# Kernel tuning notes

Hardware: AMD Instinct MI355X
Metric: run time of the kernel (lower is better)

## Reference

```python
import jax, jax.numpy as jnp
import numpy as np

BSZ = 2048
L = 64            # sequence length, power of 2
D = 15            # symbol_repr_size
NC = 10           # n_classes; embedding row NC is the 'inf' token
TREE_LEN = 2 * L - 1  # next_power_of_2(L)*2 - 1


def rms_norm(x):
    # x / (sqrt(mean(x^2, -1) + 1e-6) + 1e-6)
    return x / (jnp.sqrt(jnp.mean(x * x, axis=-1, keepdims=True) + 1e-6) + 1e-6)


def setup_inputs() -> dict:
    key = jax.random.key(0)
    k1, k2, k3, k4, k5 = jax.random.split(key, 5)
    x = jax.random.randint(k1, (BSZ, L), 0, NC)
    q = jnp.sort(jax.random.randint(k2, (BSZ, 2), 0, L), axis=1)  # low <= high
    query_low, query_high = q[:, 0], q[:, 1]
    emb = jax.random.normal(k3, (NC + 1, D), dtype=jnp.float32)
    W_lin = jax.random.normal(k4, (NC, D), dtype=jnp.float32) * 0.26   # ~1/sqrt(D)
    W_rule = jax.random.normal(k5, (2, D * D), dtype=jnp.float32) * 0.066  # ~1/D
    return {"emb": emb, "W_lin": W_lin, "W_rule": W_rule,
            "x": x, "query_low": query_low, "query_high": query_high}


def reference(emb, W_lin, W_rule, x, query_low, query_high):
    def combine(a, b):
        # outer product [b, D, D] -> rule linear (225 -> 2) -> softmax mix
        inp = jnp.einsum('bi,bj->bij', a, b).reshape(a.shape[0], -1)
        alpha = jax.nn.softmax(inp @ W_rule.T, axis=-1)  # [b, 2]
        return alpha[:, :1] * a + alpha[:, 1:] * b

    def build(trees, lst, low, high, pos):
        # recursive segment-tree build; low/high/pos are static Python ints
        if low == high:
            return rms_norm(trees.at[:, pos, :].set(lst[:, low, :]))
        mid = (low + high) // 2
        trees = build(trees, lst, low, mid, 2 * pos + 1)
        trees = build(trees, lst, mid + 1, high, 2 * pos + 2)
        mix = combine(trees[:, 2 * pos + 1], trees[:, 2 * pos + 2])
        return rms_norm(trees.at[:, pos, :].set(mix))

    inf_raw = emb[NC]  # raw inf token used inside query (no rms_norm in torch)

    def query(trees, returns, low, high, pos):
        if pos >= TREE_LEN:
            return returns
        f = returns.dtype
        mA = ((query_low <= low) & (query_high >= high)).astype(f)[:, None]
        returns = mA * trees[:, pos] + (1 - mA) * returns
        mB = ((query_low > high) | (query_high < low)).astype(f)[:, None]
        returns = mB * inf_raw[None, :] + (1 - mB) * returns
        mC = (1 - mA) * (1 - mB)
        mid = (low + high) // 2
        a1 = query(trees, returns, low, mid, 2 * pos + 1)
        a2 = query(trees, returns, mid + 1, high, 2 * pos + 2)
        new = combine(a1, a2)
        return rms_norm(mC * new + (1 - mC) * returns)

    h = rms_norm(emb[x])                              # [BSZ, L, D]
    inf_n = rms_norm(emb[NC][None, None, :])          # normalized inf token
    trees = jnp.broadcast_to(inf_n, (BSZ, TREE_LEN, D)) + jnp.zeros((), emb.dtype)
    trees = build(trees, h, 0, L - 1, 0)              # [BSZ, TREE_LEN, D]
    returns = jnp.zeros((BSZ, D), dtype=emb.dtype)
    returns = query(trees, returns, 0, L - 1, 0)      # [BSZ, D]
    return returns @ W_lin.T                          # [BSZ, NC]
```

## Files before the change

### kernel.cpp

```cpp
#include <hip/hip_runtime.h>
#include <math.h>

#define DD 15
#define DP 20
#define LL 64
#define NCC 10
#define TL 127

__device__ __forceinline__ float dpp_xor1(float x) {
    return __int_as_float(__builtin_amdgcn_update_dpp(0, __float_as_int(x), 177, 0xF, 0xF, true));
}
__device__ __forceinline__ float dpp_xor2(float x) {
    return __int_as_float(__builtin_amdgcn_update_dpp(0, __float_as_int(x), 78, 0xF, 0xF, true));
}
__device__ __forceinline__ float swz_xor4(float x) {
    return __int_as_float(__builtin_amdgcn_ds_swizzle(__float_as_int(x), 0x101F));
}

__device__ __forceinline__ float fast_rcp(float x)  { return __builtin_amdgcn_rcpf(x); }
__device__ __forceinline__ float fast_sqrt(float x) { return __builtin_amdgcn_sqrtf(x); }

__device__ __forceinline__ void combine8(const float (*tree)[DP], const float w[4][DD],
                                         int k, int qr, int u, int p,
                                         float& v0, float& v1, float& inv)
{
    const float* Lrow = &tree[2 * p + 1][0];
    const float* Rrow = &tree[2 * p + 2][0];
    float4 R0 = ((const float4*)Rrow)[0];
    float4 R1 = ((const float4*)Rrow)[1];
    float4 R2 = ((const float4*)Rrow)[2];
    float4 R3 = ((const float4*)Rrow)[3];
    float4 Aq = ((const float4*)Lrow)[qr];
    float Bv[DD] = {R0.x,R0.y,R0.z,R0.w, R1.x,R1.y,R1.z,R1.w,
                    R2.x,R2.y,R2.z,R2.w, R3.x,R3.y,R3.z};
    float Av[4] = {Aq.x, Aq.y, Aq.z, Aq.w};

    float acc = 0.f;
    #pragma unroll
    for (int ri = 0; ri < 4; ++ri) {
        float d0 = 0.f;
        #pragma unroll
        for (int j = 0; j < DD; ++j) d0 = fmaf(w[ri][j], Bv[j], d0);
        acc = fmaf(Av[ri], d0, acc);
    }
    acc += dpp_xor2(acc);
    acc += swz_xor4(acc);
    float oth = dpp_xor1(acc);
    float mx = fmaxf(acc, oth);
    float es = __expf(acc - mx), eo = __expf(oth - mx);
    float rs = fast_rcp(es + eo);
    float aS = es * rs, aO = eo * rs;
    float a0 = (k == 0) ? aS : aO;
    float a1 = (k == 0) ? aO : aS;

    float2 lm = ((const float2*)Lrow)[u];
    float2 rm = ((const float2*)Rrow)[u];
    v0 = a0 * lm.x + a1 * rm.x;
    v1 = a0 * lm.y + a1 * rm.y;
    float ss = v0 * v0 + v1 * v1;
    ss += dpp_xor1(ss);
    ss += dpp_xor2(ss);
    ss += swz_xor4(ss);
    inv = fast_rcp(fast_sqrt(ss * (1.0f / DD) + 1e-6f) + 1e-6f);
}

template<int LVL, bool QUERY>
__device__ __forceinline__ void do_level(float (*tree)[DP], const float (*nemb)[DP],
                                         const float w[4][DD], int t, int ql, int qh)
{
    constexpr int n = 1 << LVL, first = n - 1, nst = (n + 7) / 8, s = LL >> LVL;
    const int k = t & 1, qr = (t >> 1) & 3, u = t & 7, g = t >> 3;
    #pragma unroll
    for (int st = 0; st < nst; ++st) {
        int pi0 = st * 8 + g;
        int pi = (pi0 < n) ? pi0 : (n - 1);
        int p = first + pi;
        float v0, v1, inv;
        combine8(tree, w, k, qr, u, p, v0, v1, inv);
        if constexpr (!QUERY) {
            if (pi0 < n)
                ((float2*)&tree[p][0])[u] = make_float2(v0 * inv, v1 * inv);
        } else {
            int lo = pi * s, hi = lo + s - 1;
            bool full = (ql <= lo) && (qh >= hi);
            bool disj = (ql > hi) || (qh < lo);
            if (pi0 < n && !full) {
                float2 wv;
                if (disj) wv = ((const float2*)&nemb[NCC][0])[u];
                else      wv = make_float2(v0 * inv, v1 * inv);
                ((float2*)&tree[p][0])[u] = wv;
            }
        }
    }
    __syncthreads();
}

extern "C" __global__ __attribute__((amdgpu_flat_work_group_size(64, 64)))
void seg_tree_kernel(
    const float* __restrict__ emb,
    const float* __restrict__ W_lin,
    const float* __restrict__ W_rule,
    const int*  __restrict__ x,
    const int*  __restrict__ qlo_g,
    const int*  __restrict__ qhi_g,
    float* __restrict__ out)
{
    __shared__ __align__(16) float nemb[NCC + 1][DP];
    __shared__ __align__(16) float tree[TL][DP];

    const int t = threadIdx.x;
    const int b = blockIdx.x;
    const int k = t & 1, qr = (t >> 1) & 3;

    float w[4][DD];
    #pragma unroll
    for (int ri = 0; ri < 4; ++ri) {
        int i = 4 * qr + ri;
        bool valid = (i < DD);
        const float* src = W_rule + k * DD * DD + (valid ? i * DD : 0);
        #pragma unroll
        for (int j = 0; j < DD; ++j) w[ri][j] = valid ? src[j] : 0.0f;
    }

    if (t < NCC + 1) {
        float v[DD]; float ssum = 0.f;
        #pragma unroll
        for (int d = 0; d < DD; ++d) { v[d] = emb[t * DD + d]; ssum += v[d] * v[d]; }
        float inv = fast_rcp(fast_sqrt(ssum * (1.0f / DD) + 1e-6f) + 1e-6f);
        #pragma unroll
        for (int d = 0; d < DD; ++d) nemb[t][d] = v[d] * inv;
        nemb[t][DD] = 0.0f;
    }
    __syncthreads();

    {
        int xi = x[b * LL + t];
        #pragma unroll
        for (int j = 0; j < 4; ++j)
            ((float4*)&tree[63 + t][0])[j] = ((const float4*)&nemb[xi][0])[j];
    }
    __syncthreads();

    do_level<5, false>(tree, nemb, w, t, 0, 0);
    do_level<4, false>(tree, nemb, w, t, 0, 0);
    do_level<3, false>(tree, nemb, w, t, 0, 0);
    do_level<2, false>(tree, nemb, w, t, 0, 0);
    do_level<1, false>(tree, nemb, w, t, 0, 0);
    do_level<0, false>(tree, nemb, w, t, 0, 0);

    const int ql = qlo_g[b], qh = qhi_g[b];
    {
        bool inr = (ql <= t) && (qh >= t);
        if (!inr) {
            #pragma unroll
            for (int j = 0; j < 4; ++j)
                ((float4*)&tree[63 + t][0])[j] = ((const float4*)&nemb[NCC][0])[j];
        }
    }
    __syncthreads();

    do_level<5, true>(tree, nemb, w, t, ql, qh);
    do_level<4, true>(tree, nemb, w, t, ql, qh);
    do_level<3, true>(tree, nemb, w, t, ql, qh);
    do_level<2, true>(tree, nemb, w, t, ql, qh);
    do_level<1, true>(tree, nemb, w, t, ql, qh);
    do_level<0, true>(tree, nemb, w, t, ql, qh);

    if (t < NCC) {
        float acc = 0.f;
        #pragma unroll
        for (int d = 0; d < DD; ++d) acc = fmaf(tree[0][d], W_lin[t * DD + d], acc);
        out[b * NCC + t] = acc;
    }
}

extern "C" void kernel_launch(void* const* d_in, const int* in_sizes, int n_in,
                              void* d_out, int out_size, void* d_ws, size_t ws_size,
                              hipStream_t stream) {
    const float* emb    = (const float*)d_in[0];
    const float* W_lin  = (const float*)d_in[1];
    const float* W_rule = (const float*)d_in[2];
    const int*   x      = (const int*)d_in[3];
    const int*   qlo    = (const int*)d_in[4];
    const int*   qhi    = (const int*)d_in[5];
    float* outp = (float*)d_out;

    int bsz = in_sizes[3] / LL;
    seg_tree_kernel<<<dim3(bsz), dim3(64), 0, stream>>>(
        emb, W_lin, W_rule, x, qlo, qhi, outp);
}
```

Before: 18.83 us.

## Query only the two boundary paths and interleave query with build levels

The query phase now works only on the two tree paths that touch the query boundaries, with one path per 8-lane group. It no longer recombines every node at every level, and the query levels run alongside later build levels to share barriers, which cuts the number of __syncthreads. Disjoint children read the inf token directly instead of writing it into tree leaves. The ds_swizzle cross-lane ops become DPP row-mirror ops, and rcp(sqrt) becomes rsq, which drops the +1e-6 outer epsilon and may change numerics slightly. W_lin is also preloaded into registers. The main risk is correctness in the boundary-path logic and the ordering of overwritten tree nodes.

```diff
diff --git a/kernel.cpp b/kernel.cpp
--- a/kernel.cpp
+++ b/kernel.cpp
@@ -8,24 +8,19 @@
 #define TL 127
 
 __device__ __forceinline__ float dpp_xor1(float x) {
-    return __int_as_float(__builtin_amdgcn_update_dpp(0, __float_as_int(x), 177, 0xF, 0xF, true));
+    return __int_as_float(__builtin_amdgcn_update_dpp(0, __float_as_int(x), 0xB1, 0xF, 0xF, true));
 }
 __device__ __forceinline__ float dpp_xor2(float x) {
-    return __int_as_float(__builtin_amdgcn_update_dpp(0, __float_as_int(x), 78, 0xF, 0xF, true));
-}
-__device__ __forceinline__ float swz_xor4(float x) {
-    return __int_as_float(__builtin_amdgcn_ds_swizzle(__float_as_int(x), 0x101F));
-}
-
-__device__ __forceinline__ float fast_rcp(float x)  { return __builtin_amdgcn_rcpf(x); }
-__device__ __forceinline__ float fast_sqrt(float x) { return __builtin_amdgcn_sqrtf(x); }
-
-__device__ __forceinline__ void combine8(const float (*tree)[DP], const float w[4][DD],
-                                         int k, int qr, int u, int p,
-                                         float& v0, float& v1, float& inv)
-{
-    const float* Lrow = &tree[2 * p + 1][0];
-    const float* Rrow = &tree[2 * p + 2][0];
+    return __int_as_float(__builtin_amdgcn_update_dpp(0, __float_as_int(x), 0x4E, 0xF, 0xF, true));
+}
+__device__ __forceinline__ float dpp_hmirror(float x) {
+    return __int_as_float(__builtin_amdgcn_update_dpp(0, __float_as_int(x), 0x141, 0xF, 0xF, true));
+}
+
+__device__ __forceinline__ void combine8_core(const float* Lrow, const float* Rrow,
+                                              const float w[4][DD], int k, int qr, int u,
+                                              float& o0, float& o1)
+{
     float4 R0 = ((const float4*)Rrow)[0];
     float4 R1 = ((const float4*)Rrow)[1];
     float4 R2 = ((const float4*)Rrow)[2];
@@ -35,64 +30,81 @@
                     R2.x,R2.y,R2.z,R2.w, R3.x,R3.y,R3.z};
     float Av[4] = {Aq.x, Aq.y, Aq.z, Aq.w};
 
-    float acc = 0.f;
+    float p = 0.f;
     #pragma unroll
     for (int ri = 0; ri < 4; ++ri) {
         float d0 = 0.f;
         #pragma unroll
         for (int j = 0; j < DD; ++j) d0 = fmaf(w[ri][j], Bv[j], d0);
-        acc = fmaf(Av[ri], d0, acc);
-    }
-    acc += dpp_xor2(acc);
-    acc += swz_xor4(acc);
-    float oth = dpp_xor1(acc);
-    float mx = fmaxf(acc, oth);
-    float es = __expf(acc - mx), eo = __expf(oth - mx);
-    float rs = fast_rcp(es + eo);
+        p = fmaf(Av[ri], d0, p);
+    }
+    float a   = p + dpp_xor2(p);
+    float hma = dpp_hmirror(a);
+    float self = a + dpp_xor1(hma);
+    float oth  = dpp_xor1(a) + hma;
+    float mx = fmaxf(self, oth);
+    float es = __expf(self - mx), eo = __expf(oth - mx);
+    float rs = __builtin_amdgcn_rcpf(es + eo);
     float aS = es * rs, aO = eo * rs;
     float a0 = (k == 0) ? aS : aO;
     float a1 = (k == 0) ? aO : aS;
 
     float2 lm = ((const float2*)Lrow)[u];
     float2 rm = ((const float2*)Rrow)[u];
-    v0 = a0 * lm.x + a1 * rm.x;
-    v1 = a0 * lm.y + a1 * rm.y;
+    float v0 = a0 * lm.x + a1 * rm.x;
+    float v1 = a0 * lm.y + a1 * rm.y;
     float ss = v0 * v0 + v1 * v1;
     ss += dpp_xor1(ss);
     ss += dpp_xor2(ss);
-    ss += swz_xor4(ss);
-    inv = fast_rcp(fast_sqrt(ss * (1.0f / DD) + 1e-6f) + 1e-6f);
-}
-
-template<int LVL, bool QUERY>
-__device__ __forceinline__ void do_level(float (*tree)[DP], const float (*nemb)[DP],
-                                         const float w[4][DD], int t, int ql, int qh)
-{
-    constexpr int n = 1 << LVL, first = n - 1, nst = (n + 7) / 8, s = LL >> LVL;
-    const int k = t & 1, qr = (t >> 1) & 3, u = t & 7, g = t >> 3;
+    ss += dpp_hmirror(ss);
+    float inv = __builtin_amdgcn_rsqf(ss * (1.0f / DD) + 1e-6f);
+    o0 = v0 * inv; o1 = v1 * inv;
+}
+
+template<int LVL>
+__device__ __forceinline__ void build_level(float (*tree)[DP], const float w[4][DD],
+                                            int k, int qr, int u, int g)
+{
+    constexpr int n = 1 << LVL, first = n - 1, nst = (n + 7) / 8;
     #pragma unroll
     for (int st = 0; st < nst; ++st) {
         int pi0 = st * 8 + g;
-        int pi = (pi0 < n) ? pi0 : (n - 1);
+        int pi = (n < 8) ? ((pi0 < n) ? pi0 : 0) : pi0;
         int p = first + pi;
-        float v0, v1, inv;
-        combine8(tree, w, k, qr, u, p, v0, v1, inv);
-        if constexpr (!QUERY) {
-            if (pi0 < n)
-                ((float2*)&tree[p][0])[u] = make_float2(v0 * inv, v1 * inv);
-        } else {
-            int lo = pi * s, hi = lo + s - 1;
-            bool full = (ql <= lo) && (qh >= hi);
-            bool disj = (ql > hi) || (qh < lo);
-            if (pi0 < n && !full) {
-                float2 wv;
-                if (disj) wv = ((const float2*)&nemb[NCC][0])[u];
-                else      wv = make_float2(v0 * inv, v1 * inv);
-                ((float2*)&tree[p][0])[u] = wv;
-            }
-        }
-    }
-    __syncthreads();
+        float o0, o1;
+        combine8_core(&tree[2 * p + 1][0], &tree[2 * p + 2][0], w, k, qr, u, o0, o1);
+        if (pi0 < n)
+            ((float2*)&tree[p][0])[u] = make_float2(o0, o1);
+    }
+}
+
+template<int LVL>
+__device__ __forceinline__ void query_level(float (*tree)[DP], const float (*nemb)[DP],
+                                            const float w[4][DD], int t, int k, int qr, int u,
+                                            int ql, int qh)
+{
+    constexpr int first = (1 << LVL) - 1;
+    constexpr int sh = 6 - LVL;
+    constexpr int shc = sh - 1;
+    const int g2 = (t >> 3) & 1;
+    int bnd = g2 ? qh : ql;
+    int pi = bnd >> sh;
+    int lo = pi << sh, hi = lo + (1 << sh) - 1;
+    bool full = (ql <= lo) && (qh >= hi);
+    int p = first + pi;
+    int ci1 = 2 * pi, ci2 = 2 * pi + 1;
+    int lo1 = ci1 << shc, hi1 = lo1 + (1 << shc) - 1;
+    int lo2 = ci2 << shc, hi2 = lo2 + (1 << shc) - 1;
+    bool d1 = (ql > hi1) || (qh < lo1);
+    bool d2 = (ql > hi2) || (qh < lo2);
+    const float* Lrow = d1 ? &nemb[NCC][0] : &tree[2 * p + 1][0];
+    const float* Rrow = d2 ? &nemb[NCC][0] : &tree[2 * p + 2][0];
+    float o0, o1;
+    combine8_core(Lrow, Rrow, w, k, qr, u, o0, o1);
+    int pi_g0 = ql >> sh;
+    bool we = (!full) && (t < 16) && (g2 == 0 || pi != pi_g0);
+    if (we)
+        ((float2*)&tree[p][0])[u] = make_float2(o0, o1);
 }
 
 extern "C" __global__ __attribute__((amdgpu_flat_work_group_size(64, 64)))
@@ -110,7 +122,10 @@
 
     const int t = threadIdx.x;
     const int b = blockIdx.x;
-    const int k = t & 1, qr = (t >> 1) & 3;
+    const int k = t & 1, qr = (t >> 1) & 3, u = t & 7, g = t >> 3;
+
+    const int xi = x[b * LL + t];
+    const int ql = qlo_g[b], qh = qhi_g[b];
 
     float w[4][DD];
     #pragma unroll
@@ -121,55 +136,61 @@
         #pragma unroll
         for (int j = 0; j < DD; ++j) w[ri][j] = valid ? src[j] : 0.0f;
     }
+    #pragma unroll
+    for (int ri = 0; ri < 4; ++ri)
+        #pragma unroll
+        for (int j = 0; j < DD; ++j)
+            asm volatile("" : "+v"(w[ri][j]));
+
+    float wl[DD];
+    {
+        const float* wlp = W_lin + ((t < NCC) ? t : 0) * DD;
+        #pragma unroll
+        for (int d = 0; d < DD; ++d) wl[d] = wlp[d];
+        #pragma unroll
+        for (int d = 0; d < DD; ++d) asm volatile("" : "+v"(wl[d]));
+    }
 
     if (t < NCC + 1) {
         float v[DD]; float ssum = 0.f;
         #pragma unroll
         for (int d = 0; d < DD; ++d) { v[d] = emb[t * DD + d]; ssum += v[d] * v[d]; }
-        float inv = fast_rcp(fast_sqrt(ssum * (1.0f / DD) + 1e-6f) + 1e-6f);
+        float inv = __builtin_amdgcn_rsqf(ssum * (1.0f / DD) + 1e-6f);
         #pragma unroll
         for (int d = 0; d < DD; ++d) nemb[t][d] = v[d] * inv;
         nemb[t][DD] = 0.0f;
     }
     __syncthreads();
 
-    {
-        int xi = x[b * LL + t];
-        #pragma unroll
-        for (int j = 0; j < 4; ++j)
-            ((float4*)&tree[63 + t][0])[j] = ((const float4*)&nemb[xi][0])[j];
-    }
-    __syncthreads();
-
-    do_level<5, false>(tree, nemb, w, t, 0, 0);
-    do_level<4, false>(tree, nemb, w, t, 0, 0);
-    do_level<3, false>(tree, nemb, w, t, 0, 0);
-    do_level<2, false>(tree, nemb, w, t, 0, 0);
-    do_level<1, false>(tree, nemb, w, t, 0, 0);
-    do_level<0, false>(tree, nemb, w, t, 0, 0);
-
-    const int ql = qlo_g[b], qh = qhi_g[b];
-    {
-        bool inr = (ql <= t) && (qh >= t);
-        if (!inr) {
-            #pragma unroll
-            for (int j = 0; j < 4; ++j)
-                ((float4*)&tree[63 + t][0])[j] = ((const float4*)&nemb[NCC][0])[j];
-        }
-    }
-    __syncthreads();
-
-    do_level<5, true>(tree, nemb, w, t, ql, qh);
-    do_level<4, true>(tree, nemb, w, t, ql, qh);
-    do_level<3, true>(tree, nemb, w, t, ql, qh);
-    do_level<2, true>(tree, nemb, w, t, ql, qh);
-    do_level<1, true>(tree, nemb, w, t, ql, qh);
-    do_level<0, true>(tree, nemb, w, t, ql, qh);
+    #pragma unroll
+    for (int j = 0; j < 4; ++j)
+        ((float4*)&tree[63 + t][0])[j] = ((const float4*)&nemb[xi][0])[j];
+    __syncthreads();
+
+    build_level<5>(tree, w, k, qr, u, g);
+    __syncthreads();
+    build_level<4>(tree, w, k, qr, u, g);
+    query_level<5>(tree, nemb, w, t, k, qr, u, ql, qh);
+    __syncthreads();
+    build_level<3>(tree, w, k, qr, u, g);
+    query_level<4>(tree, nemb, w, t, k, qr, u, ql, qh);
+    __syncthreads();
+    build_level<2>(tree, w, k, qr, u, g);
+    query_level<3>(tree, nemb, w, t, k, qr, u, ql, qh);
+    __syncthreads();
+    build_level<1>(tree, w, k, qr, u, g);
+    query_level<2>(tree, nemb, w, t, k, qr, u, ql, qh);
+    __syncthreads();
+    build_level<0>(tree, w, k, qr, u, g);
+    query_level<1>(tree, nemb, w, t, k, qr, u, ql, qh);
+    __syncthreads();
+    query_level<0>(tree, nemb, w, t, k, qr, u, ql, qh);
+    __syncthreads();
 
     if (t < NCC) {
         float acc = 0.f;
         #pragma unroll
-        for (int d = 0; d < DD; ++d) acc = fmaf(tree[0][d], W_lin[t * DD + d], acc);
+        for (int d = 0; d < DD; ++d) acc = fmaf(tree[0][d], wl[d], acc);
         out[b * NCC + t] = acc;
     }
 }
```

Result: faster. 16.33 us (-13.3%).
